# Optimization experiments

Hardware: AMD Instinct MI355X
Metric: run time of the kernel (lower is better)

The kernel has to match this reference:

```python
import jax, jax.numpy as jnp
import numpy as np

NUM_HEADS = 4
WORD_DIM = 100
LEAKY_ALPHA = 0.3  # keras LeakyReLU default negative_slope


def setup_inputs() -> dict:
    key = jax.random.key(0)
    k1, k2, k3 = jax.random.split(key, 3)
    x = jax.random.normal(k1, (8, 30, 20, 40, WORD_DIM), dtype=jnp.float32)
    # keras 'random_normal' initializer: stddev 0.05
    w_att = jax.random.normal(k2, (NUM_HEADS, WORD_DIM), dtype=jnp.float32) * 0.05
    b_att = jax.random.normal(k3, (NUM_HEADS, WORD_DIM), dtype=jnp.float32) * 0.05
    return {"x": x, "w_att": w_att, "b_att": b_att}


def reference(x, w_att, b_att):
    # x: [B, T, E, W, D]; w_att, b_att: [H, D]
    B, T, E, W, D = x.shape
    H = w_att.shape[0]
    type_emb = x[..., 0, :]        # [B,T,E,D]
    words = x[..., 1:, :]          # [B,T,E,N,D], N = W-1
    # per-head hidden representation: leaky_relu(w*words + b)
    pre = words[..., None, :, :] * w_att[:, None, :] + b_att[:, None, :]  # [B,T,E,H,N,D]
    hidden = jnp.where(pre >= 0, pre, LEAKY_ALPHA * pre)
    # attention scores: dot(type_emb, hidden) over D
    scores = jnp.einsum('bted,btehnd->btehn', type_emb, hidden)  # [B,T,E,H,N]
    # original uses raw exp / sum (no max-subtraction) -- keep faithful
    att = jnp.exp(scores)
    att = att / jnp.sum(att, axis=-1, keepdims=True)
    out = jnp.einsum('btehn,btend->bthed'.replace('bthed', 'btehd'), att, words)  # [B,T,E,H,D]
    out = out.reshape(B, T, E, H * D)
    # all-zero events map to zero embeddings
    nonzero = jnp.any(x != 0, axis=(-1, -2), keepdims=False)  # [B,T,E]
    out = jnp.where(nonzero[..., None], out, 0.0)
    return out
```

## Files before the change

kernel.cpp:

```cpp
#include <hip/hip_runtime.h>
#include <math.h>
#include <stdint.h>

#define NHEAD 4
#define DD 100
#define NW 39
#define BLOCK 256

typedef float v2f __attribute__((ext_vector_type(2)));
typedef __attribute__((address_space(3))) uint32_t lds_t;
typedef const __attribute__((address_space(1))) uint32_t glb_t;

__global__ __launch_bounds__(BLOCK, 6) void ts_enc(
    const float* __restrict__ x,
    const float* __restrict__ w_att,
    const float* __restrict__ b_att,
    float* __restrict__ out)
{
    __shared__ float tile[40 * DD];
    __shared__ float scp[NHEAD][4][40];

    const int tid  = threadIdx.x;
    const int wv   = __builtin_amdgcn_readfirstlane(tid >> 6);
    const int lane = tid & 63;
    const float* xsite = x + (size_t)blockIdx.x * (40 * DD);

    #pragma unroll
    for (int i = 0; i < 4; ++i) {
        const int cf = i * BLOCK + tid;
        if (cf < 1000) {
            glb_t* g = (glb_t*)(xsite + cf * 4);
            lds_t* l = (lds_t*)(tile + (i * BLOCK + wv * 64) * 4);
            __builtin_amdgcn_global_load_lds(g, l, 16, 0, 0);
        }
    }
    __syncthreads();

    const bool act  = lane < NW;
    const int  nrow = act ? lane : NW - 1;
    const float* wrow = tile + (1 + nrow) * DD;

    v2f accA[NHEAD] = {{0,0},{0,0},{0,0},{0,0}};
    v2f accB[NHEAD] = {{0,0},{0,0},{0,0},{0,0}};

#define ABODY(cc) { \
        const int c_ = (cc); \
        const v2f x01 = *(const v2f*)(wrow + c_ * 4); \
        const v2f x23 = *(const v2f*)(wrow + c_ * 4 + 2); \
        const v2f t01 = *(const v2f*)(tile + c_ * 4); \
        const v2f t23 = *(const v2f*)(tile + c_ * 4 + 2); \
        _Pragma("unroll") \
        for (int h = 0; h < NHEAD; ++h) { \
            const v2f w01 = *(const v2f*)(w_att + h * DD + c_ * 4); \
            const v2f w23 = *(const v2f*)(w_att + h * DD + c_ * 4 + 2); \
            const v2f b01 = *(const v2f*)(b_att + h * DD + c_ * 4); \
            const v2f b23 = *(const v2f*)(b_att + h * DD + c_ * 4 + 2); \
            const v2f p01 = x01 * w01 + b01; \
            const v2f p23 = x23 * w23 + b23; \
            const v2f l01 = __builtin_elementwise_max(p01, 0.3f * p01); \
            const v2f l23 = __builtin_elementwise_max(p23, 0.3f * p23); \
            accA[h] = t01 * l01 + accA[h]; \
            accB[h] = t23 * l23 + accB[h]; \
        } }

    #pragma unroll
    for (int j = 0; j < 6; ++j) ABODY(wv * 6 + j)
    if (wv == 0) ABODY(24)
#undef ABODY

    if (act) {
        #pragma unroll
        for (int h = 0; h < NHEAD; ++h)
            scp[h][wv][lane] = (accA[h].x + accA[h].y) + (accB[h].x + accB[h].y);
    }
    __syncthreads();

    float sc = 0.f;
    if (act) sc = (scp[wv][0][lane] + scp[wv][1][lane])
                + (scp[wv][2][lane] + scp[wv][3][lane]);
    const float e = act ? __expf(sc) : 0.f;
    float sm = e;
    #pragma unroll
    for (int off = 32; off; off >>= 1) sm += __shfl_xor(sm, off);
    const float att = e / sm;

    const int l2 = lane < 50 ? lane : 49;
    const float* wb = tile + DD + l2 * 2;
    float ox = 0.f, oy = 0.f;
    #pragma unroll
    for (int n = 0; n < NW; ++n) {
        const float attn = __builtin_bit_cast(float,
            __builtin_amdgcn_readlane(__builtin_bit_cast(int, att), n));
        const v2f wd = *(const v2f*)(wb + n * DD);
        ox = fmaf(attn, wd.x, ox);
        oy = fmaf(attn, wd.y, oy);
    }
    if (lane < 50) {
        const v2f o = {ox, oy};
        *(v2f*)(out + (size_t)blockIdx.x * (NHEAD * DD) + wv * DD + lane * 2) = o;
    }
}

extern "C" void kernel_launch(void* const* d_in, const int* in_sizes, int n_in,
                              void* d_out, int out_size, void* d_ws, size_t ws_size,
                              hipStream_t stream) {
    const float* x     = (const float*)d_in[0];
    const float* w_att = (const float*)d_in[1];
    const float* b_att = (const float*)d_in[2];
    float* out = (float*)d_out;

    const int sites = 8 * 30 * 20;
    ts_enc<<<sites, BLOCK, 0, stream>>>(x, w_att, b_att, out);
}
```

Before: 27.50 us.

## Split softmax/weighted-sum across two waves and read type embedding from global

```diff
diff --git a/kernel.cpp b/kernel.cpp
--- a/kernel.cpp
+++ b/kernel.cpp
@@ -18,7 +18,7 @@
     float* __restrict__ out)
 {
     __shared__ float tile[40 * DD];
-    __shared__ float scp[NHEAD][4][40];
+    __shared__ float scp2[4][40][4];
 
     const int tid  = threadIdx.x;
     const int wv   = __builtin_amdgcn_readfirstlane(tid >> 6);
@@ -47,8 +47,8 @@
         const int c_ = (cc); \
         const v2f x01 = *(const v2f*)(wrow + c_ * 4); \
         const v2f x23 = *(const v2f*)(wrow + c_ * 4 + 2); \
-        const v2f t01 = *(const v2f*)(tile + c_ * 4); \
-        const v2f t23 = *(const v2f*)(tile + c_ * 4 + 2); \
+        const v2f t01 = *(const v2f*)(xsite + c_ * 4);        \
+        const v2f t23 = *(const v2f*)(xsite + c_ * 4 + 2); \
         _Pragma("unroll") \
         for (int h = 0; h < NHEAD; ++h) { \
             const v2f w01 = *(const v2f*)(w_att + h * DD + c_ * 4); \
@@ -69,35 +69,51 @@
 #undef ABODY
 
     if (act) {
-        #pragma unroll
-        for (int h = 0; h < NHEAD; ++h)
-            scp[h][wv][lane] = (accA[h].x + accA[h].y) + (accB[h].x + accB[h].y);
+        float4 sc4;
+        sc4.x = accA[0].x + accA[0].y + accB[0].x + accB[0].y;
+        sc4.y = accA[1].x + accA[1].y + accB[1].x + accB[1].y;
+        sc4.z = accA[2].x + accA[2].y + accB[2].x + accB[2].y;
+        sc4.w = accA[3].x + accA[3].y + accB[3].x + accB[3].y;
+        *(float4*)&scp2[wv][lane][0] = sc4;
     }
     __syncthreads();
 
-    float sc = 0.f;
-    if (act) sc = (scp[wv][0][lane] + scp[wv][1][lane])
-                + (scp[wv][2][lane] + scp[wv][3][lane]);
-    const float e = act ? __expf(sc) : 0.f;
-    float sm = e;
-    #pragma unroll
-    for (int off = 32; off; off >>= 1) sm += __shfl_xor(sm, off);
-    const float att = e / sm;
+    const int role = (wv + blockIdx.x) & 3;
+    if (role >= 2) return;
+
+    v2f s01 = {0.f, 0.f};
+    if (act) {
+        #pragma unroll
+        for (int sw = 0; sw < 4; ++sw)
+            s01 += *(const v2f*)&scp2[sw][lane][2 * role];
+    }
+    const float e0 = act ? __expf(s01.x) : 0.f;
+    const float e1 = act ? __expf(s01.y) : 0.f;
 
     const int l2 = lane < 50 ? lane : 49;
     const float* wb = tile + DD + l2 * 2;
-    float ox = 0.f, oy = 0.f;
+    v2f o0 = {0.f, 0.f}, o1 = {0.f, 0.f};
+    float s0 = 0.f, s1 = 0.f;
     #pragma unroll
     for (int n = 0; n < NW; ++n) {
-        const float attn = __builtin_bit_cast(float,
-            __builtin_amdgcn_readlane(__builtin_bit_cast(int, att), n));
         const v2f wd = *(const v2f*)(wb + n * DD);
-        ox = fmaf(attn, wd.x, ox);
-        oy = fmaf(attn, wd.y, oy);
+        const float a0 = __builtin_bit_cast(float,
+            __builtin_amdgcn_readlane(__builtin_bit_cast(int, e0), n));
+        const float a1 = __builtin_bit_cast(float,
+            __builtin_amdgcn_readlane(__builtin_bit_cast(int, e1), n));
+        o0 = a0 * wd + o0;
+        o1 = a1 * wd + o1;
+        s0 += a0;
+        s1 += a1;
     }
+    const float r0 = 1.f / s0;
+    const float r1 = 1.f / s1;
     if (lane < 50) {
-        const v2f o = {ox, oy};
-        *(v2f*)(out + (size_t)blockIdx.x * (NHEAD * DD) + wv * DD + lane * 2) = o;
+        float* ob = out + (size_t)blockIdx.x * (NHEAD * DD) + (2 * role) * DD + lane * 2;
+        const v2f q0 = o0 * r0;
+        const v2f q1 = o1 * r1;
+        *(v2f*)(ob)      = q0;
+        *(v2f*)(ob + DD) = q1;
     }
 }
 
```

Result: slower. 30.10 us (+9.4%).
